# Optimization experiments

Measured on AMD Instinct MI355X. Metric: run time of the kernel, lower is better.

## Reference

```python
import jax, jax.numpy as jnp
import numpy as np

N_EMBD = 1024
N_HEADS = 16
HEAD_DIM = N_EMBD // N_HEADS


def setup_inputs() -> dict:
    key = jax.random.key(0)
    ks = jax.random.split(key, 12)
    B, T, S, C = 2, 2048, 2048, N_EMBD
    std = 1.0 / np.sqrt(C)
    inp = {
        "x": jax.random.normal(ks[0], (B, T, C), dtype=jnp.float32),
        "context": jax.random.normal(ks[1], (B, S, C), dtype=jnp.float32),
        "q_w": jax.random.uniform(ks[2], (C, C), minval=-std, maxval=std, dtype=jnp.float32),
        "q_b": jax.random.uniform(ks[3], (C,), minval=-std, maxval=std, dtype=jnp.float32),
        "k_w": jax.random.uniform(ks[4], (C, C), minval=-std, maxval=std, dtype=jnp.float32),
        "k_b": jax.random.uniform(ks[5], (C,), minval=-std, maxval=std, dtype=jnp.float32),
        "v_w": jax.random.uniform(ks[6], (C, C), minval=-std, maxval=std, dtype=jnp.float32),
        "v_b": jax.random.uniform(ks[7], (C,), minval=-std, maxval=std, dtype=jnp.float32),
        "o_w": jax.random.uniform(ks[8], (C, C), minval=-std, maxval=std, dtype=jnp.float32),
        "o_b": jax.random.uniform(ks[9], (C,), minval=-std, maxval=std, dtype=jnp.float32),
    }
    return inp


def reference(x, context, q_w, q_b, k_w, k_b, v_w, v_b, o_w, o_b):
    B, T, C = x.shape
    S = context.shape[1]
    H, D = N_HEADS, HEAD_DIM
    # projections (torch Linear: y = x @ W^T + b; here weights stored as [in, out])
    q = (x @ q_w + q_b).reshape(B, T, H, D).transpose(0, 2, 1, 3)        # [B,H,T,D]
    k = (context @ k_w + k_b).reshape(B, S, H, D).transpose(0, 2, 1, 3)  # [B,H,S,D]
    v = (context @ v_w + v_b).reshape(B, S, H, D).transpose(0, 2, 1, 3)  # [B,H,S,D]
    att = jnp.einsum("bhtd,bhsd->bhts", q, k) / jnp.sqrt(jnp.float32(D))  # [B,H,T,S]
    causal = jnp.tril(jnp.ones((T, S), dtype=bool))                       # mask from tril buffer
    att = jnp.where(causal[None, None, :, :], att, -jnp.inf)
    att = jax.nn.softmax(att, axis=-1)
    y = jnp.einsum("bhts,bhsd->bhtd", att, v)                             # [B,H,T,D]
    y = y.transpose(0, 2, 1, 3).reshape(B, T, C)
    return y @ o_w + o_b
```

## Files before the change

kernel.cpp:

```cpp
#include <hip/hip_runtime.h>
#include <hip/hip_bf16.h>

using bf16 = __bf16;
using bf16x4 = __attribute__((ext_vector_type(4))) __bf16;
using bf16x8 = __attribute__((ext_vector_type(8))) __bf16;
using f32x4 = __attribute__((ext_vector_type(4))) float;
using u32 = unsigned int;

#define EXP2F(x) __builtin_amdgcn_exp2f(x)

__device__ __forceinline__ void gload16(const void* g, void* l) {
  __builtin_amdgcn_global_load_lds((const __attribute__((address_space(1))) u32*)g,
                                   (__attribute__((address_space(3))) u32*)l, 16, 0, 0);
}

__global__ __launch_bounds__(256) void prep_kernel(const float4* __restrict__ x4,
                                                   const float4* __restrict__ c4,
                                                   bf16x4* __restrict__ xb4,
                                                   const float* __restrict__ w0,
                                                   const float* __restrict__ w1,
                                                   const float* __restrict__ w2,
                                                   const float* __restrict__ w3,
                                                   bf16* __restrict__ wtbase) {
  __shared__ float tile[32][33];
  const int bid = blockIdx.x;
  const int tid = threadIdx.x;
  if (bid < 8192) {
    int g = bid * 256 + tid;
    float4 v = (g < 1048576) ? x4[g] : c4[g - 1048576];
    bf16x4 o = {(bf16)v.x, (bf16)v.y, (bf16)v.z, (bf16)v.w};
    xb4[g] = o;
  } else {
    const int t = bid - 8192;
    const int z = t >> 10, rem = t & 1023;
    const int n0 = (rem & 31) * 32, k0 = (rem >> 5) * 32;
    const float* w = (z == 0) ? w0 : (z == 1) ? w1 : (z == 2) ? w2 : w3;
    bf16* wt = wtbase + (size_t)z * 1048576;
    const int tx = tid & 31, ty = tid >> 5;
#pragma unroll
    for (int i = 0; i < 4; i++)
      tile[ty + i * 8][tx] = w[(size_t)(k0 + ty + i * 8) * 1024 + n0 + tx];
    __syncthreads();
#pragma unroll
    for (int i = 0; i < 4; i++)
      wt[(size_t)(n0 + ty + i * 8) * 1024 + k0 + tx] = (bf16)tile[tx][ty + i * 8];
  }
}

template <int MODE>
__device__ __forceinline__ void gemm_body(char* __restrict__ smem,
                                          const bf16* __restrict__ A,
                                          const bf16* __restrict__ Bt,
                                          const float* __restrict__ bias,
                                          void* __restrict__ outp, int bx, int by,
                                          float oscale) {
  constexpr int K = 1024;
  bf16(*Cs)[136] = (bf16(*)[136])smem;

  const int tid = threadIdx.x;
  const int lane = tid & 63;
  const int w = tid >> 6;
  const int wr = w >> 1, wc = w & 1;
  const int m0 = by * 128, n0 = bx * 128;
  const int fr = lane & 15, lg = lane >> 4;

  const int p = lane & 3;
  const int r0 = w * 16 + (lane >> 2);
  const int r1 = r0 + 64;
  const char* gA0 = (const char*)(A + (size_t)(m0 + r0) * K) + ((p ^ ((r0 >> 1) & 3)) << 4);
  const char* gA1 = (const char*)(A + (size_t)(m0 + r1) * K) + ((p ^ ((r1 >> 1) & 3)) << 4);
  const char* gB0 = (const char*)(Bt + (size_t)(n0 + r0) * K) + ((p ^ ((r0 >> 1) & 3)) << 4);
  const char* gB1 = (const char*)(Bt + (size_t)(n0 + r1) * K) + ((p ^ ((r1 >> 1) & 3)) << 4);

  const int sA = (fr >> 1) & 3;
  int aoff[4], boff[4];
#pragma unroll
  for (int mi = 0; mi < 4; mi++)
    aoff[mi] = (wr * 64 + mi * 16 + fr) * 64 + ((lg ^ sA) << 4);
#pragma unroll
  for (int ni = 0; ni < 4; ni++)
    boff[ni] = 8192 + (wc * 64 + ni * 16 + fr) * 64 + ((lg ^ sA) << 4);

  f32x4 acc[4][4] = {};

  auto stage = [&](int t, int buf) {
    char* b = smem + buf * 16384;
    const int go = t * 64;
    gload16(gA0 + go, b + w * 1024);
    gload16(gA1 + go, b + 4096 + w * 1024);
    gload16(gB0 + go, b + 8192 + w * 1024);
    gload16(gB1 + go, b + 12288 + w * 1024);
  };

  stage(0, 0);
  stage(1, 1);

  int cb = 0;
  for (int it = 0; it < 32; ++it) {
    if (it < 31)
      asm volatile("s_waitcnt vmcnt(4)" ::: "memory");
    else
      asm volatile("s_waitcnt vmcnt(0)" ::: "memory");
    __builtin_amdgcn_s_barrier();
    __builtin_amdgcn_sched_barrier(0);
    if (it + 2 < 32) {
      int nb = cb - 1;
      if (nb < 0) nb = 2;
      stage(it + 2, nb);
    }
    const char* base = smem + cb * 16384;
    bf16x8 af[4], bfr[4];
#pragma unroll
    for (int mi = 0; mi < 4; mi++) af[mi] = *(const bf16x8*)(base + aoff[mi]);
#pragma unroll
    for (int ni = 0; ni < 4; ni++) bfr[ni] = *(const bf16x8*)(base + boff[ni]);
#pragma unroll
    for (int mi = 0; mi < 4; mi++)
#pragma unroll
      for (int ni = 0; ni < 4; ni++)
        acc[mi][ni] =
            __builtin_amdgcn_mfma_f32_16x16x32_bf16(af[mi], bfr[ni], acc[mi][ni], 0, 0, 0);
    cb = (cb == 2) ? 0 : cb + 1;
  }

  asm volatile("" ::: "memory");
  float bv[4];
#pragma unroll
  for (int ni = 0; ni < 4; ni++) bv[ni] = bias[n0 + wc * 64 + ni * 16 + fr];
#pragma unroll
  for (int mi = 0; mi < 4; mi++)
#pragma unroll
    for (int ni = 0; ni < 4; ni++)
#pragma unroll
      for (int j = 0; j < 4; j++) acc[mi][ni][j] = (acc[mi][ni][j] + bv[ni]) * oscale;

  if (MODE == 2) {
    float* O = (float*)outp;
#pragma unroll
    for (int mi = 0; mi < 4; mi++)
#pragma unroll
      for (int ni = 0; ni < 4; ni++)
#pragma unroll
        for (int j = 0; j < 4; j++) {
          int row = m0 + wr * 64 + mi * 16 + (lane >> 4) * 4 + j;
          int col = n0 + wc * 64 + ni * 16 + fr;
          O[(size_t)row * 1024 + col] = acc[mi][ni][j];
        }
    return;
  }

  __syncthreads();
#pragma unroll
  for (int mi = 0; mi < 4; mi++) {
    int r = wr * 64 + mi * 16 + (lane >> 4) * 4;
#pragma unroll
    for (int ni = 0; ni < 4; ni++) {
      int c = wc * 64 + ni * 16 + fr;
#pragma unroll
      for (int j = 0; j < 4; j++) Cs[r + j][c] = (bf16)acc[mi][ni][j];
    }
  }
  __syncthreads();

  bf16* O = (bf16*)outp;
  if (MODE == 0) {
    int row = tid >> 1, ch = (tid & 1) * 64;
    int rg = m0 + row;
    int b = rg >> 11, t_ = rg & 2047;
    int c0 = n0 + ch;
    int h = c0 >> 6;
    bf16* dst = O + ((size_t)(b * 16 + h) * 2048 + t_) * 64;
#pragma unroll
    for (int i = 0; i < 8; i++) *(bf16x8*)&dst[i * 8] = *(const bf16x8*)&Cs[row][ch + i * 8];
  } else {
    int colL = tid >> 1, sh = (tid & 1) * 64;
    int cg = n0 + colL;
    int h = cg >> 6, d = cg & 63;
    int rg = m0 + sh;
    int b = rg >> 11, s_ = rg & 2047;
    bf16* dst = O + ((size_t)((b * 16 + h) * 64 + d)) * 2048 + s_;
#pragma unroll
    for (int i = 0; i < 8; i++) {
      bf16x8 v;
#pragma unroll
      for (int jj = 0; jj < 8; jj++) v[jj] = Cs[sh + i * 8 + jj][colL];
      *(bf16x8*)&dst[i * 8] = v;
    }
  }
}

__global__ __launch_bounds__(256) void gemm_qkv_kernel(const bf16* __restrict__ xb,
                                                       const bf16* __restrict__ cb,
                                                       const bf16* __restrict__ wtbase,
                                                       const float* __restrict__ bq,
                                                       const float* __restrict__ bk,
                                                       const float* __restrict__ bv,
                                                       bf16* __restrict__ outbase) {
  __shared__ __align__(16) char smem[49152];
  const int lin = blockIdx.x;
  const int xcd = lin & 7, idx = lin >> 3;
  const int seq = xcd * 96 + idx;
  const int z = seq >> 8;
  const int rem = seq & 255;
  const int by = rem >> 3, bx = rem & 7;
  const bf16* A = (z == 0) ? xb : cb;
  const bf16* Wt = wtbase + (size_t)z * 1048576;
  const float* bias = (z == 0) ? bq : (z == 1) ? bk : bv;
  bf16* out = outbase + (size_t)z * 4194304;
  const float oscale = (z == 0) ? 0.125f * 1.4426950408889634f : 1.0f;
  if (z == 2)
    gemm_body<1>(smem, A, Wt, bias, (void*)out, bx, by, oscale);
  else
    gemm_body<0>(smem, A, Wt, bias, (void*)out, bx, by, oscale);
}

__global__ __launch_bounds__(256) void gemm_o_kernel(const bf16* __restrict__ A,
                                                     const bf16* __restrict__ Wt,
                                                     const float* __restrict__ bias,
                                                     float* __restrict__ out) {
  __shared__ __align__(16) char smem[49152];
  const int lin = blockIdx.x;
  const int xcd = lin & 7, idx = lin >> 3;
  const int seq = xcd * 32 + idx;
  const int by = seq >> 3, bx = seq & 7;
  gemm_body<2>(smem, A, Wt, bias, (void*)out, bx, by, 1.0f);
}

__global__ __launch_bounds__(256) void attn_kernel(const bf16* __restrict__ Q,
                                                   const bf16* __restrict__ Kc,
                                                   const bf16* __restrict__ Vt,
                                                   bf16* __restrict__ Y) {
  const int bh = blockIdx.x;
  const int qt = 31 - blockIdx.y;
  const int tid = threadIdx.x, lane = tid & 63, w = tid >> 6;
  const int lr = lane & 15, lg = lane >> 4;
  const int q0 = qt * 64 + w * 16;

  __shared__ __align__(16) bf16 Ks[64 * 64];
  __shared__ __align__(16) bf16 Vs[64 * 64];
  __shared__ __align__(16) bf16 Plds[4][16][72];

  const bf16* qb = Q + ((size_t)bh * 2048 + q0 + lr) * 64 + lg * 8;
  const bf16x8 qfB0 = *(const bf16x8*)qb;
  const bf16x8 qfB1 = *(const bf16x8*)(qb + 32);

  const bf16* Kbase = Kc + (size_t)bh * 2048 * 64;
  const bf16* Vbase = Vt + (size_t)bh * 64 * 2048;

  const int srow = tid >> 2;
  const int scol = (tid & 3) * 16;
  const int r7x = (srow & 7) * 8;
  const int d0 = srow * 64 + (scol ^ r7x);
  const int d1 = srow * 64 + ((scol + 8) ^ r7x);

  bf16x8 kr0, kr1, vr0, vr1;
  {
    const bf16* kp = Kbase + (size_t)srow * 64 + scol;
    kr0 = *(const bf16x8*)kp;
    kr1 = *(const bf16x8*)(kp + 8);
    const bf16* vp = Vbase + (size_t)srow * 2048 + scol;
    vr0 = *(const bf16x8*)vp;
    vr1 = *(const bf16x8*)(vp + 8);
  }

  f32x4 yacc[4] = {};
  float mrow = -__builtin_inff(), lrow = 0.0f;
  const int kxor = (lr & 7) * 8;

  for (int c = 0; c <= qt; ++c) {
    const int sbase = c * 64;
    __syncthreads();
    *(bf16x8*)&Ks[d0] = kr0;
    *(bf16x8*)&Ks[d1] = kr1;
    *(bf16x8*)&Vs[d0] = vr0;
    *(bf16x8*)&Vs[d1] = vr1;
    __syncthreads();

    {
      const int cn = (c < qt) ? c + 1 : c;
      const int sb = cn * 64;
      const bf16* kp = Kbase + (size_t)(sb + srow) * 64 + scol;
      kr0 = *(const bf16x8*)kp;
      kr1 = *(const bf16x8*)(kp + 8);
      const bf16* vp = Vbase + (size_t)srow * 2048 + sb + scol;
      vr0 = *(const bf16x8*)vp;
      vr1 = *(const bf16x8*)(vp + 8);
    }

    f32x4 st[4];
    __builtin_amdgcn_s_setprio(1);
#pragma unroll
    for (int h = 0; h < 4; ++h) {
      const int rb = (16 * h + lr) * 64;
      const bf16x8 kf0 = *(const bf16x8*)&Ks[rb + ((lg * 8) ^ kxor)];
      const bf16x8 kf1 = *(const bf16x8*)&Ks[rb + ((32 + lg * 8) ^ kxor)];
      f32x4 z = {};
      z = __builtin_amdgcn_mfma_f32_16x16x32_bf16(kf0, qfB0, z, 0, 0, 0);
      z = __builtin_amdgcn_mfma_f32_16x16x32_bf16(kf1, qfB1, z, 0, 0, 0);
      st[h] = z;
    }
    __builtin_amdgcn_s_setprio(0);
    if (c == qt) {
      const int qg = q0 + lr;
#pragma unroll
      for (int h = 0; h < 4; ++h)
#pragma unroll
        for (int j = 0; j < 4; ++j) {
          int sg = sbase + 16 * h + lg * 4 + j;
          if (sg > qg) st[h][j] = -__builtin_inff();
        }
    }
    float vmax = fmaxf(fmaxf(st[0][0], st[0][1]), fmaxf(st[0][2], st[0][3]));
#pragma unroll
    for (int h = 1; h < 4; ++h)
      vmax = fmaxf(vmax, fmaxf(fmaxf(st[h][0], st[h][1]), fmaxf(st[h][2], st[h][3])));
    vmax = fmaxf(vmax, __shfl_xor(vmax, 16));
    vmax = fmaxf(vmax, __shfl_xor(vmax, 32));

    if (!__all(vmax <= mrow)) {
      const float mnew = fmaxf(mrow, vmax);
      const float cf = EXP2F(mrow - mnew);
      mrow = mnew;
      lrow *= cf;
      float cfj[4];
#pragma unroll
      for (int j = 0; j < 4; ++j) cfj[j] = __shfl(cf, lg * 4 + j);
#pragma unroll
      for (int nf = 0; nf < 4; ++nf)
#pragma unroll
        for (int j = 0; j < 4; ++j) yacc[nf][j] *= cfj[j];
    }

    float rs = 0.0f;
#pragma unroll
    for (int h = 0; h < 4; ++h) {
      float p0 = EXP2F(st[h][0] - mrow);
      float p1 = EXP2F(st[h][1] - mrow);
      float p2 = EXP2F(st[h][2] - mrow);
      float p3 = EXP2F(st[h][3] - mrow);
      rs += (p0 + p1) + (p2 + p3);
      bf16x4 pk = {(bf16)p0, (bf16)p1, (bf16)p2, (bf16)p3};
      *(bf16x4*)&Plds[w][lr][16 * h + lg * 4] = pk;
    }
    rs += __shfl_xor(rs, 16);
    rs += __shfl_xor(rs, 32);
    lrow += rs;

    const bf16x8 pa0 = *(const bf16x8*)&Plds[w][lr][lg * 8];
    const bf16x8 pa1 = *(const bf16x8*)&Plds[w][lr][32 + lg * 8];
    __builtin_amdgcn_s_setprio(1);
#pragma unroll
    for (int nf = 0; nf < 4; ++nf) {
      const int rb = (nf * 16 + lr) * 64;
      const bf16x8 vf0 = *(const bf16x8*)&Vs[rb + ((lg * 8) ^ kxor)];
      const bf16x8 vf1 = *(const bf16x8*)&Vs[rb + ((32 + lg * 8) ^ kxor)];
      yacc[nf] = __builtin_amdgcn_mfma_f32_16x16x32_bf16(pa0, vf0, yacc[nf], 0, 0, 0);
      yacc[nf] = __builtin_amdgcn_mfma_f32_16x16x32_bf16(pa1, vf1, yacc[nf], 0, 0, 0);
    }
    __builtin_amdgcn_s_setprio(0);
  }

  const float rinv = 1.0f / lrow;
  float linv[4];
#pragma unroll
  for (int j = 0; j < 4; ++j) linv[j] = __shfl(rinv, lg * 4 + j);
  const int b = bh >> 4, h = bh & 15;
#pragma unroll
  for (int nf = 0; nf < 4; ++nf)
#pragma unroll
    for (int j = 0; j < 4; ++j) {
      int qg = q0 + lg * 4 + j;
      Y[((size_t)b * 2048 + qg) * 1024 + h * 64 + nf * 16 + lr] = (bf16)(yacc[nf][j] * linv[j]);
    }
}

extern "C" void kernel_launch(void* const* d_in, const int* in_sizes, int n_in,
                              void* d_out, int out_size, void* d_ws, size_t ws_size,
                              hipStream_t stream) {
  const float* x = (const float*)d_in[0];
  const float* ctx = (const float*)d_in[1];
  const float* q_w = (const float*)d_in[2];
  const float* q_b = (const float*)d_in[3];
  const float* k_w = (const float*)d_in[4];
  const float* k_b = (const float*)d_in[5];
  const float* v_w = (const float*)d_in[6];
  const float* v_b = (const float*)d_in[7];
  const float* o_w = (const float*)d_in[8];
  const float* o_b = (const float*)d_in[9];

  char* ws = (char*)d_ws;
  const size_t MB = 1024 * 1024;
  bf16* xb = (bf16*)(ws + 0);
  bf16* qwt = (bf16*)(ws + 16 * MB);
  bf16* Qws = (bf16*)(ws + 24 * MB);
  bf16* Kws = (bf16*)(ws + 32 * MB);
  bf16* Vt = (bf16*)(ws + 40 * MB);
  bf16* Yws = (bf16*)(ws + 48 * MB);
  bf16* owt = qwt + 3 * 1048576;
  bf16* cb = xb + 4194304;

  prep_kernel<<<12288, 256, 0, stream>>>((const float4*)x, (const float4*)ctx, (bf16x4*)xb,
                                         q_w, k_w, v_w, o_w, qwt);

  gemm_qkv_kernel<<<768, 256, 0, stream>>>(xb, cb, qwt, q_b, k_b, v_b, Qws);

  attn_kernel<<<dim3(32, 32), 256, 0, stream>>>(Qws, Kws, Vt, Yws);

  gemm_o_kernel<<<256, 256, 0, stream>>>(Yws, owt, o_b, (float*)d_out);
}
```

Baseline: 111.5 us.

## Pair complementary causal query tiles per attention block for load balance

Each attention block now handles two query tiles, ytile and 31-ytile, one after the other. Every block then does the same total amount of causal work, and the grid is halved to 32x16. The goal is to remove the tail imbalance from uneven per-tile causal work. The cost is half as many blocks, which may reduce occupancy and latency hiding on a GPU with 256 CUs.

```diff
diff --git a/kernel.cpp b/kernel.cpp
--- a/kernel.cpp
+++ b/kernel.cpp
@@ -231,18 +231,13 @@
                                                    const bf16* __restrict__ Vt,
                                                    bf16* __restrict__ Y) {
   const int bh = blockIdx.x;
-  const int qt = 31 - blockIdx.y;
+  const int ytile = blockIdx.y;
   const int tid = threadIdx.x, lane = tid & 63, w = tid >> 6;
   const int lr = lane & 15, lg = lane >> 4;
-  const int q0 = qt * 64 + w * 16;
 
   __shared__ __align__(16) bf16 Ks[64 * 64];
   __shared__ __align__(16) bf16 Vs[64 * 64];
   __shared__ __align__(16) bf16 Plds[4][16][72];
-
-  const bf16* qb = Q + ((size_t)bh * 2048 + q0 + lr) * 64 + lg * 8;
-  const bf16x8 qfB0 = *(const bf16x8*)qb;
-  const bf16x8 qfB1 = *(const bf16x8*)(qb + 32);
 
   const bf16* Kbase = Kc + (size_t)bh * 2048 * 64;
   const bf16* Vbase = Vt + (size_t)bh * 64 * 2048;
@@ -252,126 +247,137 @@
   const int r7x = (srow & 7) * 8;
   const int d0 = srow * 64 + (scol ^ r7x);
   const int d1 = srow * 64 + ((scol + 8) ^ r7x);
-
-  bf16x8 kr0, kr1, vr0, vr1;
-  {
-    const bf16* kp = Kbase + (size_t)srow * 64 + scol;
-    kr0 = *(const bf16x8*)kp;
-    kr1 = *(const bf16x8*)(kp + 8);
-    const bf16* vp = Vbase + (size_t)srow * 2048 + scol;
-    vr0 = *(const bf16x8*)vp;
-    vr1 = *(const bf16x8*)(vp + 8);
-  }
-
-  f32x4 yacc[4] = {};
-  float mrow = -__builtin_inff(), lrow = 0.0f;
   const int kxor = (lr & 7) * 8;
-
-  for (int c = 0; c <= qt; ++c) {
-    const int sbase = c * 64;
-    __syncthreads();
-    *(bf16x8*)&Ks[d0] = kr0;
-    *(bf16x8*)&Ks[d1] = kr1;
-    *(bf16x8*)&Vs[d0] = vr0;
-    *(bf16x8*)&Vs[d1] = vr1;
-    __syncthreads();
-
+  const int b = bh >> 4, h = bh & 15;
+
+#pragma unroll 1
+  for (int pass = 0; pass < 2; ++pass) {
+    const int qt = (pass == 0) ? ytile : 31 - ytile;
+    const int q0 = qt * 64 + w * 16;
+
+    const bf16* qb = Q + ((size_t)bh * 2048 + q0 + lr) * 64 + lg * 8;
+    const bf16x8 qfB0 = *(const bf16x8*)qb;
+    const bf16x8 qfB1 = *(const bf16x8*)(qb + 32);
+
+    bf16x8 kr0, kr1, vr0, vr1;
     {
-      const int cn = (c < qt) ? c + 1 : c;
-      const int sb = cn * 64;
-      const bf16* kp = Kbase + (size_t)(sb + srow) * 64 + scol;
+      const bf16* kp = Kbase + (size_t)srow * 64 + scol;
       kr0 = *(const bf16x8*)kp;
       kr1 = *(const bf16x8*)(kp + 8);
-      const bf16* vp = Vbase + (size_t)srow * 2048 + sb + scol;
+      const bf16* vp = Vbase + (size_t)srow * 2048 + scol;
       vr0 = *(const bf16x8*)vp;
       vr1 = *(const bf16x8*)(vp + 8);
     }
 
-    f32x4 st[4];
-    __builtin_amdgcn_s_setprio(1);
-#pragma unroll
-    for (int h = 0; h < 4; ++h) {
-      const int rb = (16 * h + lr) * 64;
-      const bf16x8 kf0 = *(const bf16x8*)&Ks[rb + ((lg * 8) ^ kxor)];
-      const bf16x8 kf1 = *(const bf16x8*)&Ks[rb + ((32 + lg * 8) ^ kxor)];
-      f32x4 z = {};
-      z = __builtin_amdgcn_mfma_f32_16x16x32_bf16(kf0, qfB0, z, 0, 0, 0);
-      z = __builtin_amdgcn_mfma_f32_16x16x32_bf16(kf1, qfB1, z, 0, 0, 0);
-      st[h] = z;
+    f32x4 yacc[4] = {};
+    float mrow = -__builtin_inff(), lrow = 0.0f;
+
+    for (int c = 0; c <= qt; ++c) {
+      const int sbase = c * 64;
+      __syncthreads();
+      *(bf16x8*)&Ks[d0] = kr0;
+      *(bf16x8*)&Ks[d1] = kr1;
+      *(bf16x8*)&Vs[d0] = vr0;
+      *(bf16x8*)&Vs[d1] = vr1;
+      __syncthreads();
+
+      {
+        const int cn = (c < qt) ? c + 1 : c;
+        const int sb = cn * 64;
+        const bf16* kp = Kbase + (size_t)(sb + srow) * 64 + scol;
+        kr0 = *(const bf16x8*)kp;
+        kr1 = *(const bf16x8*)(kp + 8);
+        const bf16* vp = Vbase + (size_t)srow * 2048 + sb + scol;
+        vr0 = *(const bf16x8*)vp;
+        vr1 = *(const bf16x8*)(vp + 8);
+      }
+
+      f32x4 st[4];
+      __builtin_amdgcn_s_setprio(1);
+#pragma unroll
+      for (int hh = 0; hh < 4; ++hh) {
+        const int rb = (16 * hh + lr) * 64;
+        const bf16x8 kf0 = *(const bf16x8*)&Ks[rb + ((lg * 8) ^ kxor)];
+        const bf16x8 kf1 = *(const bf16x8*)&Ks[rb + ((32 + lg * 8) ^ kxor)];
+        f32x4 z = {};
+        z = __builtin_amdgcn_mfma_f32_16x16x32_bf16(kf0, qfB0, z, 0, 0, 0);
+        z = __builtin_amdgcn_mfma_f32_16x16x32_bf16(kf1, qfB1, z, 0, 0, 0);
+        st[hh] = z;
+      }
+      __builtin_amdgcn_s_setprio(0);
+      if (c == qt) {
+        const int qg = q0 + lr;
+#pragma unroll
+        for (int hh = 0; hh < 4; ++hh)
+#pragma unroll
+          for (int j = 0; j < 4; ++j) {
+            int sg = sbase + 16 * hh + lg * 4 + j;
+            if (sg > qg) st[hh][j] = -__builtin_inff();
+          }
+      }
+      float vmax = fmaxf(fmaxf(st[0][0], st[0][1]), fmaxf(st[0][2], st[0][3]));
+#pragma unroll
+      for (int hh = 1; hh < 4; ++hh)
+        vmax = fmaxf(vmax, fmaxf(fmaxf(st[hh][0], st[hh][1]), fmaxf(st[hh][2], st[hh][3])));
+      vmax = fmaxf(vmax, __shfl_xor(vmax, 16));
+      vmax = fmaxf(vmax, __shfl_xor(vmax, 32));
+
+      if (!__all(vmax <= mrow)) {
+        const float mnew = fmaxf(mrow, vmax);
+        const float cf = EXP2F(mrow - mnew);
+        mrow = mnew;
+        lrow *= cf;
+        float cfj[4];
+#pragma unroll
+        for (int j = 0; j < 4; ++j) cfj[j] = __shfl(cf, lg * 4 + j);
+#pragma unroll
+        for (int nf = 0; nf < 4; ++nf)
+#pragma unroll
+          for (int j = 0; j < 4; ++j) yacc[nf][j] *= cfj[j];
+      }
+
+      float rs = 0.0f;
+#pragma unroll
+      for (int hh = 0; hh < 4; ++hh) {
+        float p0 = EXP2F(st[hh][0] - mrow);
+        float p1 = EXP2F(st[hh][1] - mrow);
+        float p2 = EXP2F(st[hh][2] - mrow);
+        float p3 = EXP2F(st[hh][3] - mrow);
+        rs += (p0 + p1) + (p2 + p3);
+        bf16x4 pk = {(bf16)p0, (bf16)p1, (bf16)p2, (bf16)p3};
+        *(bf16x4*)&Plds[w][lr][16 * hh + lg * 4] = pk;
+      }
+      rs += __shfl_xor(rs, 16);
+      rs += __shfl_xor(rs, 32);
+      lrow += rs;
+
+      const bf16x8 pa0 = *(const bf16x8*)&Plds[w][lr][lg * 8];
+      const bf16x8 pa1 = *(const bf16x8*)&Plds[w][lr][32 + lg * 8];
+      __builtin_amdgcn_s_setprio(1);
+#pragma unroll
+      for (int nf = 0; nf < 4; ++nf) {
+        const int rb = (nf * 16 + lr) * 64;
+        const bf16x8 vf0 = *(const bf16x8*)&Vs[rb + ((lg * 8) ^ kxor)];
+        const bf16x8 vf1 = *(const bf16x8*)&Vs[rb + ((32 + lg * 8) ^ kxor)];
+        yacc[nf] = __builtin_amdgcn_mfma_f32_16x16x32_bf16(pa0, vf0, yacc[nf], 0, 0, 0);
+        yacc[nf] = __builtin_amdgcn_mfma_f32_16x16x32_bf16(pa1, vf1, yacc[nf], 0, 0, 0);
+      }
+      __builtin_amdgcn_s_setprio(0);
     }
-    __builtin_amdgcn_s_setprio(0);
-    if (c == qt) {
-      const int qg = q0 + lr;
-#pragma unroll
-      for (int h = 0; h < 4; ++h)
-#pragma unroll
-        for (int j = 0; j < 4; ++j) {
-          int sg = sbase + 16 * h + lg * 4 + j;
-          if (sg > qg) st[h][j] = -__builtin_inff();
-        }
-    }
-    float vmax = fmaxf(fmaxf(st[0][0], st[0][1]), fmaxf(st[0][2], st[0][3]));
-#pragma unroll
-    for (int h = 1; h < 4; ++h)
-      vmax = fmaxf(vmax, fmaxf(fmaxf(st[h][0], st[h][1]), fmaxf(st[h][2], st[h][3])));
-    vmax = fmaxf(vmax, __shfl_xor(vmax, 16));
-    vmax = fmaxf(vmax, __shfl_xor(vmax, 32));
-
-    if (!__all(vmax <= mrow)) {
-      const float mnew = fmaxf(mrow, vmax);
-      const float cf = EXP2F(mrow - mnew);
-      mrow = mnew;
-      lrow *= cf;
-      float cfj[4];
-#pragma unroll
-      for (int j = 0; j < 4; ++j) cfj[j] = __shfl(cf, lg * 4 + j);
-#pragma unroll
-      for (int nf = 0; nf < 4; ++nf)
-#pragma unroll
-        for (int j = 0; j < 4; ++j) yacc[nf][j] *= cfj[j];
-    }
-
-    float rs = 0.0f;
-#pragma unroll
-    for (int h = 0; h < 4; ++h) {
-      float p0 = EXP2F(st[h][0] - mrow);
-      float p1 = EXP2F(st[h][1] - mrow);
-      float p2 = EXP2F(st[h][2] - mrow);
-      float p3 = EXP2F(st[h][3] - mrow);
-      rs += (p0 + p1) + (p2 + p3);
-      bf16x4 pk = {(bf16)p0, (bf16)p1, (bf16)p2, (bf16)p3};
-      *(bf16x4*)&Plds[w][lr][16 * h + lg * 4] = pk;
-    }
-    rs += __shfl_xor(rs, 16);
-    rs += __shfl_xor(rs, 32);
-    lrow += rs;
-
-    const bf16x8 pa0 = *(const bf16x8*)&Plds[w][lr][lg * 8];
-    const bf16x8 pa1 = *(const bf16x8*)&Plds[w][lr][32 + lg * 8];
-    __builtin_amdgcn_s_setprio(1);
-#pragma unroll
-    for (int nf = 0; nf < 4; ++nf) {
-      const int rb = (nf * 16 + lr) * 64;
-      const bf16x8 vf0 = *(const bf16x8*)&Vs[rb + ((lg * 8) ^ kxor)];
-      const bf16x8 vf1 = *(const bf16x8*)&Vs[rb + ((32 + lg * 8) ^ kxor)];
-      yacc[nf] = __builtin_amdgcn_mfma_f32_16x16x32_bf16(pa0, vf0, yacc[nf], 0, 0, 0);
-      yacc[nf] = __builtin_amdgcn_mfma_f32_16x16x32_bf16(pa1, vf1, yacc[nf], 0, 0, 0);
-    }
-    __builtin_amdgcn_s_setprio(0);
-  }
-
-  const float rinv = 1.0f / lrow;
-  float linv[4];
-#pragma unroll
-  for (int j = 0; j < 4; ++j) linv[j] = __shfl(rinv, lg * 4 + j);
-  const int b = bh >> 4, h = bh & 15;
-#pragma unroll
-  for (int nf = 0; nf < 4; ++nf)
-#pragma unroll
-    for (int j = 0; j < 4; ++j) {
-      int qg = q0 + lg * 4 + j;
-      Y[((size_t)b * 2048 + qg) * 1024 + h * 64 + nf * 16 + lr] = (bf16)(yacc[nf][j] * linv[j]);
-    }
+
+    const float rinv = 1.0f / lrow;
+    float linv[4];
+#pragma unroll
+    for (int j = 0; j < 4; ++j) linv[j] = __shfl(rinv, lg * 4 + j);
+#pragma unroll
+    for (int nf = 0; nf < 4; ++nf)
+#pragma unroll
+      for (int j = 0; j < 4; ++j) {
+        int qg = q0 + lg * 4 + j;
+        Y[((size_t)b * 2048 + qg) * 1024 + h * 64 + nf * 16 + lr] =
+            (bf16)(yacc[nf][j] * linv[j]);
+      }
+  }
 }
 
 extern "C" void kernel_launch(void* const* d_in, const int* in_sizes, int n_in,
@@ -404,7 +410,7 @@
 
   gemm_qkv_kernel<<<768, 256, 0, stream>>>(xb, cb, qwt, q_b, k_b, v_b, Qws);
 
-  attn_kernel<<<dim3(32, 32), 256, 0, stream>>>(Qws, Kws, Vt, Yws);
+  attn_kernel<<<dim3(32, 16), 256, 0, stream>>>(Qws, Kws, Vt, Yws);
 
   gemm_o_kernel<<<256, 256, 0, stream>>>(Yws, owt, o_b, (float*)d_out);
 }
```

New measurement: 116.0 us. 4.1% more time.
